# Kernel optimization log

Hardware: AMD Instinct MI355X
Metric: run time of the kernel (lower is better)

The kernel has to match this reference:

```python
import jax, jax.numpy as jnp
import numpy as np

B, S, E, H = 4, 2048, 1024, 16
D = E // H
EPS = 1e-5


def _ln(x, g, b):
    mu = jnp.mean(x, axis=-1, keepdims=True)
    var = jnp.mean(jnp.square(x - mu), axis=-1, keepdims=True)
    return (x - mu) * jax.lax.rsqrt(var + EPS) * g + b


def setup_inputs() -> dict:
    key = jax.random.key(0)
    ks = jax.random.split(key, 12)
    s = 0.02
    return {
        "inp": jax.random.normal(ks[0], (B, S, E), jnp.float32),
        "ln1_g": jnp.ones((E,), jnp.float32),
        "ln1_b": jnp.zeros((E,), jnp.float32),
        "Wq": jax.random.normal(ks[1], (E, E), jnp.float32) * s,
        "bq": jnp.zeros((E,), jnp.float32),
        "Wk": jax.random.normal(ks[2], (E, E), jnp.float32) * s,
        "bk": jnp.zeros((E,), jnp.float32),
        "Wv": jax.random.normal(ks[3], (E, E), jnp.float32) * s,
        "bv": jnp.zeros((E,), jnp.float32),
        "Wo": jax.random.normal(ks[4], (E, E), jnp.float32) * s,
        "bo": jnp.zeros((E,), jnp.float32),
        "ln2_g": jnp.ones((E,), jnp.float32),
        "ln2_b": jnp.zeros((E,), jnp.float32),
        "W1": jax.random.normal(ks[5], (E, 2 * E), jnp.float32) * s,
        "b1": jnp.zeros((2 * E,), jnp.float32),
        "W2": jax.random.normal(ks[6], (2 * E, E), jnp.float32) * s,
        "b2": jnp.zeros((E,), jnp.float32),
    }


def reference(inp, ln1_g, ln1_b, Wq, bq, Wk, bk, Wv, bv, Wo, bo,
              ln2_g, ln2_b, W1, b1, W2, b2):
    x = _ln(inp, ln1_g, ln1_b)                      # [B,S,E]
    def heads(t):
        return t.reshape(B, S, H, D).transpose(0, 2, 1, 3)  # [B,H,S,D]
    q = heads(x @ Wq + bq)
    k = heads(x @ Wk + bk)
    v = heads(x @ Wv + bv)
    scores = jnp.einsum('bhqd,bhkd->bhqk', q, k) / jnp.sqrt(jnp.float32(D))
    attn = jax.nn.softmax(scores, axis=-1)
    out = jnp.einsum('bhqk,bhkd->bhqd', attn, v)    # [B,H,S,D]
    out = out.transpose(0, 2, 1, 3).reshape(B, S, E)
    out = out @ Wo + bo                             # dropout p=1e-4 -> identity (eval)
    x = x + out                                     # NOTE: residual from normed input (as in source)
    x = _ln(x, ln2_g, ln2_b)
    mlp = jax.nn.gelu(x @ W1 + b1, approximate=False) @ W2 + b2
    return mlp + x
```

## Files before the change

kernel.cpp:

```cpp
#include <hip/hip_runtime.h>
#include <hip/hip_bf16.h>

typedef float f32x4 __attribute__((ext_vector_type(4)));
typedef __bf16 bfv8 __attribute__((ext_vector_type(8)));

constexpr int Bc = 4, Sc = 2048, Ec = 1024, Hc = 16, Dc = 64;
constexpr int Mc = Bc * Sc;

__device__ __forceinline__ uint pkbf(float lo, float hi) {
  uint r;
  asm("v_cvt_pk_bf16_f32 %0, %1, %2" : "=v"(r) : "v"(lo), "v"(hi));
  return r;
}
__device__ __forceinline__ ushort f2bf(float f) {
  __hip_bfloat16 h = __float2bfloat16(f);
  return __builtin_bit_cast(ushort, h);
}
__device__ __forceinline__ float bf2f(ushort u) {
  return __builtin_bit_cast(float, (uint)u << 16);
}

typedef __attribute__((address_space(1))) unsigned int as1_u32;
typedef __attribute__((address_space(3))) unsigned int as3_u32;
__device__ __forceinline__ void cp16(const ushort* g, ushort* l) {
  __builtin_amdgcn_global_load_lds((as1_u32*)g, (as3_u32*)l, 16, 0, 0);
}

__global__ __launch_bounds__(256) void wcvt_all_kernel(
    const float* __restrict__ Wq, const float* __restrict__ Wk,
    const float* __restrict__ Wv, const float* __restrict__ Wo,
    const float* __restrict__ W1, const float* __restrict__ W2,
    ushort* __restrict__ WqkvT, ushort* __restrict__ WoT,
    ushort* __restrict__ W1T, ushort* __restrict__ W2T) {
  int bid = blockIdx.x;
  const float* W;
  ushort* WT;
  int K, N;
  if (bid < 1024) {
    W = Wq; WT = WqkvT; K = 1024; N = 1024;
  } else if (bid < 2048) {
    W = Wk; WT = WqkvT + (size_t)1024 * 1024; K = 1024; N = 1024; bid -= 1024;
  } else if (bid < 3072) {
    W = Wv; WT = WqkvT + (size_t)2 * 1024 * 1024; K = 1024; N = 1024; bid -= 2048;
  } else if (bid < 4096) {
    W = Wo; WT = WoT; K = 1024; N = 1024; bid -= 3072;
  } else if (bid < 6144) {
    W = W1; WT = W1T; K = 1024; N = 2048; bid -= 4096;
  } else {
    W = W2; WT = W2T; K = 2048; N = 1024; bid -= 6144;
  }
  const int nbx = K / 32;
  const int k0 = (bid % nbx) * 32, n0 = (bid / nbx) * 32;
  __shared__ float t[32][33];
  int tx = threadIdx.x, ty = threadIdx.y;
#pragma unroll
  for (int i = 0; i < 32; i += 8)
    t[ty + i][tx] = W[(size_t)(k0 + ty + i) * N + n0 + tx];
  __syncthreads();
#pragma unroll
  for (int i = 0; i < 32; i += 8)
    WT[(size_t)(n0 + ty + i) * K + k0 + tx] = f2bf(t[tx][ty + i]);
}

template <int INF32>
__global__ __launch_bounds__(256) void ln_kernel(const void* in,
                                                 const float* __restrict__ g,
                                                 const float* __restrict__ bb,
                                                 ushort* ob) {
  int row = blockIdx.x;
  int t = threadIdx.x;
  float4 x;
  if constexpr (INF32) {
    x = reinterpret_cast<const float4*>((const float*)in + (size_t)row * Ec)[t];
  } else {
    uint2 u = reinterpret_cast<const uint2*>((const ushort*)in + (size_t)row * Ec)[t];
    x.x = __builtin_bit_cast(float, u.x << 16);
    x.y = __builtin_bit_cast(float, u.x & 0xFFFF0000u);
    x.z = __builtin_bit_cast(float, u.y << 16);
    x.w = __builtin_bit_cast(float, u.y & 0xFFFF0000u);
  }
  float s = x.x + x.y + x.z + x.w;
  float q = x.x * x.x + x.y * x.y + x.z * x.z + x.w * x.w;
#pragma unroll
  for (int o = 32; o > 0; o >>= 1) {
    s += __shfl_down(s, o);
    q += __shfl_down(q, o);
  }
  __shared__ float red[10];
  int wv = t >> 6;
  if ((t & 63) == 0) { red[wv] = s; red[4 + wv] = q; }
  __syncthreads();
  if (t == 0) {
    float S = red[0] + red[1] + red[2] + red[3];
    float Q = red[4] + red[5] + red[6] + red[7];
    float mu = S * (1.f / Ec);
    float var = Q * (1.f / Ec) - mu * mu;
    red[8] = mu;
    red[9] = rsqrtf(var + 1e-5f);
  }
  __syncthreads();
  float mu = red[8], rs = red[9];
  float4 gg = reinterpret_cast<const float4*>(g)[t];
  float4 b4 = reinterpret_cast<const float4*>(bb)[t];
  float4 y;
  y.x = (x.x - mu) * rs * gg.x + b4.x;
  y.y = (x.y - mu) * rs * gg.y + b4.y;
  y.z = (x.z - mu) * rs * gg.z + b4.z;
  y.w = (x.w - mu) * rs * gg.w + b4.w;
  uint2 u;
  u.x = pkbf(y.x, y.y);
  u.y = pkbf(y.z, y.w);
  reinterpret_cast<uint2*>(ob + (size_t)row * Ec)[t] = u;
}

template <int MODE>
__global__ __launch_bounds__(256, 2) void gemm_kernel(
    int M, int N, int K, const ushort* __restrict__ A,
    const ushort* __restrict__ BT, const float* __restrict__ b0,
    const ushort* __restrict__ rb, float* outF, ushort* o0, float qscale) {
  __shared__ __align__(16) ushort As[2][128 * 64];
  __shared__ __align__(16) ushort Bs[2][128 * 64];
  const int tid = threadIdx.x;
  const int lane = tid & 63, wave = tid >> 6;
  const int wr = wave >> 1, wc = wave & 1;
  const int fr = lane & 15, fq = lane >> 4;
  const int nx = gridDim.x;
  int flat = blockIdx.x + nx * blockIdx.y;
  int cpx = (nx * gridDim.y) >> 3;
  int work = (flat & 7) * cpx + (flat >> 3);
  const int n0 = (work % nx) * 128, m0 = (work / nx) * 128;

  f32x4 acc[4][4];
#pragma unroll
  for (int i = 0; i < 4; i++)
#pragma unroll
    for (int j = 0; j < 4; j++) acc[i][j] = f32x4{0.f, 0.f, 0.f, 0.f};

  const int srow = tid >> 3;
  const int sslot = tid & 7;

  auto STAGE = [&](int p, int k0) {
#pragma unroll
    for (int c = 0; c < 4; ++c) {
      int row = c * 32 + srow;
      int scol = (sslot ^ (row & 7)) * 8;
      cp16(A + (size_t)(m0 + row) * K + k0 + scol,
           &As[p][(c * 256 + wave * 64) * 8]);
      cp16(BT + (size_t)(n0 + row) * K + k0 + scol,
           &Bs[p][(c * 256 + wave * 64) * 8]);
    }
  };

  STAGE(0, 0);
  const int nt = K >> 6;
  for (int kt = 0; kt < nt; ++kt) {
    const int p = kt & 1;
    if (kt + 1 < nt) {
      STAGE(p ^ 1, (kt + 1) << 6);
      asm volatile("s_waitcnt vmcnt(8)" ::: "memory");
    } else {
      asm volatile("s_waitcnt vmcnt(0)" ::: "memory");
    }
    __builtin_amdgcn_s_barrier();
#pragma unroll
    for (int kk = 0; kk < 2; ++kk) {
      bfv8 af[4], bf[4];
#pragma unroll
      for (int m = 0; m < 4; m++) {
        int row = wr * 64 + m * 16 + fr;
        af[m] = *reinterpret_cast<const bfv8*>(
            &As[p][row * 64 + (((kk * 4 + fq) ^ (fr & 7)) * 8)]);
      }
#pragma unroll
      for (int n = 0; n < 4; n++) {
        int row = wc * 64 + n * 16 + fr;
        bf[n] = *reinterpret_cast<const bfv8*>(
            &Bs[p][row * 64 + (((kk * 4 + fq) ^ (fr & 7)) * 8)]);
      }
      __builtin_amdgcn_s_setprio(1);
#pragma unroll
      for (int m = 0; m < 4; m++)
#pragma unroll
        for (int n = 0; n < 4; n++)
          acc[m][n] =
              __builtin_amdgcn_mfma_f32_16x16x32_bf16(af[m], bf[n], acc[m][n], 0, 0, 0);
      __builtin_amdgcn_s_setprio(0);
    }
    __builtin_amdgcn_sched_barrier(0);
    __builtin_amdgcn_s_barrier();
  }

#pragma unroll
  for (int m = 0; m < 4; m++) {
#pragma unroll
    for (int n = 0; n < 4; n++) {
      const int row0 = m0 + wr * 64 + m * 16 + fq * 4;
      const int col = n0 + wc * 64 + n * 16 + fr;
      if constexpr (MODE == 0) {
        const int b = row0 >> 11, s0 = row0 & (Sc - 1);
        const int h = col >> 6, d = col & (Dc - 1);
        const float bb = b0[col];
#pragma unroll
        for (int r = 0; r < 4; r++)
          o0[(((size_t)b * Hc + h) * Sc + s0 + r) * Dc + d] =
              f2bf((acc[m][n][r] + bb) * qscale);
      } else {
        const float bb = b0[col];
#pragma unroll
        for (int r = 0; r < 4; r++) {
          int row = row0 + r;
          size_t idx = (size_t)row * N + col;
          float vacc = acc[m][n][r] + bb + bf2f(rb[idx]);
          if constexpr (MODE == 1) {
            o0[idx] = f2bf(vacc);
          } else {
            outF[idx] = vacc;
          }
        }
      }
    }
  }
}

template <int MODE>
__global__ __launch_bounds__(512, 2) void gemm256_kernel(
    int M, int N, int K, const ushort* __restrict__ A,
    const ushort* __restrict__ BT, const float* __restrict__ b0,
    const float* __restrict__ b1, ushort* o0, ushort* o1, float qscale) {
  __shared__ __align__(16) ushort As[2][256 * 64];
  __shared__ __align__(16) ushort Bs[2][256 * 64];
  const int tid = threadIdx.x;
  const int lane = tid & 63, wave = tid >> 6;
  const int wr = wave >> 2, wc = wave & 3;
  const int fr = lane & 15, fq = lane >> 4;
  const int nx = gridDim.x;
  int flat = blockIdx.x + nx * blockIdx.y;
  int cpx = (nx * gridDim.y) >> 3;
  int work = (flat & 7) * cpx + (flat >> 3);
  const int n0 = (work % nx) * 256, m0 = (work / nx) * 256;

  f32x4 acc[8][4];
#pragma unroll
  for (int i = 0; i < 8; i++)
#pragma unroll
    for (int j = 0; j < 4; j++) acc[i][j] = f32x4{0.f, 0.f, 0.f, 0.f};

  const int srow = tid >> 3;
  const int sslot = tid & 7;

  auto STAGE = [&](int p, int k0) {
#pragma unroll
    for (int c = 0; c < 4; ++c) {
      int row = c * 64 + srow;
      int scol = (sslot ^ (row & 7)) * 8;
      cp16(A + (size_t)(m0 + row) * K + k0 + scol,
           &As[p][(c * 64 + wave * 8) * 64]);
      cp16(BT + (size_t)(n0 + row) * K + k0 + scol,
           &Bs[p][(c * 64 + wave * 8) * 64]);
    }
  };

  STAGE(0, 0);
  const int nt = K >> 6;
  for (int kt = 0; kt < nt; ++kt) {
    const int p = kt & 1;
    if (kt + 1 < nt) {
      STAGE(p ^ 1, (kt + 1) << 6);
      asm volatile("s_waitcnt vmcnt(8)" ::: "memory");
    } else {
      asm volatile("s_waitcnt vmcnt(0)" ::: "memory");
    }
    __builtin_amdgcn_s_barrier();
#pragma unroll
    for (int kk = 0; kk < 2; ++kk) {
      bfv8 bfr[4];
#pragma unroll
      for (int n = 0; n < 4; ++n) {
        int row = wc * 64 + n * 16 + fr;
        bfr[n] = *reinterpret_cast<const bfv8*>(
            &Bs[p][row * 64 + (((kk * 4 + fq) ^ (row & 7)) * 8)]);
      }
#pragma unroll
      for (int mh = 0; mh < 2; ++mh) {
        bfv8 af[4];
#pragma unroll
        for (int mm = 0; mm < 4; ++mm) {
          int row = wr * 128 + (mh * 4 + mm) * 16 + fr;
          af[mm] = *reinterpret_cast<const bfv8*>(
              &As[p][row * 64 + (((kk * 4 + fq) ^ (row & 7)) * 8)]);
        }
        __builtin_amdgcn_s_setprio(1);
#pragma unroll
        for (int mm = 0; mm < 4; ++mm)
#pragma unroll
          for (int n = 0; n < 4; ++n)
            acc[mh * 4 + mm][n] = __builtin_amdgcn_mfma_f32_16x16x32_bf16(
                af[mm], bfr[n], acc[mh * 4 + mm][n], 0, 0, 0);
        __builtin_amdgcn_s_setprio(0);
        if (!(kk == 1 && mh == 1)) __builtin_amdgcn_s_barrier();
      }
    }
    __builtin_amdgcn_sched_barrier(0);
    __builtin_amdgcn_s_barrier();
  }

#pragma unroll
  for (int m = 0; m < 8; m++) {
#pragma unroll
    for (int n = 0; n < 4; n++) {
      const int row0 = m0 + wr * 128 + m * 16 + fq * 4;
      const int col = n0 + wc * 64 + n * 16 + fr;
      if constexpr (MODE == 2) {
        const float bb = b0[col];
#pragma unroll
        for (int r = 0; r < 4; r++) {
          float vacc = acc[m][n][r] + bb;
          vacc = 0.5f * vacc * (1.f + erff(vacc * 0.70710678118f));
          o0[(size_t)(row0 + r) * N + col] = f2bf(vacc);
        }
      } else {
        const int region = col >> 10, c1 = col & (Ec - 1);
        const int b = row0 >> 11, s0 = row0 & (Sc - 1);
        const int h = c1 >> 6, d = c1 & (Dc - 1);
        const float bb = (region ? b1 : b0)[c1];
        if (region == 1) {
          uint2 u;
          u.x = pkbf(acc[m][n][0] + bb, acc[m][n][1] + bb);
          u.y = pkbf(acc[m][n][2] + bb, acc[m][n][3] + bb);
          *reinterpret_cast<uint2*>(
              &o1[(((size_t)b * Hc + h) * Dc + d) * Sc + s0]) = u;
        } else {
#pragma unroll
          for (int r = 0; r < 4; r++)
            o0[(((size_t)b * Hc + h) * Sc + s0 + r) * Dc + d] =
                f2bf(acc[m][n][r] + bb);
        }
      }
    }
  }
}

__global__ __launch_bounds__(512) void attn_kernel(const ushort* __restrict__ q,
                                                   const ushort* __restrict__ k,
                                                   const ushort* __restrict__ vt,
                                                   ushort* __restrict__ o) {
  int flat = blockIdx.x;
  int swz = (flat & 7) * 128 + (flat >> 3);
  const int qb = swz & 15;
  const int bh = swz >> 4;
  const int tid = threadIdx.x, lane = tid & 63, wave = tid >> 6;
  const int fr = lane & 15, fq = lane >> 4;
  const size_t base = (size_t)bh * Sc * Dc;
  const int q0 = qb * 128 + wave * 16;

  __shared__ __align__(16) ushort Ks[2][128 * 64];
  __shared__ __align__(16) ushort Vt[2][64 * 128];
  __shared__ __align__(16) ushort Ps[8][16 * 64];

  bfv8 qf0, qf1;
  {
    const ushort* qp = q + base + (size_t)(q0 + fr) * Dc + fq * 8;
    qf0 = *reinterpret_cast<const bfv8*>(qp);
    qf1 = *reinterpret_cast<const bfv8*>(qp + 32);
  }

  const bfv8 ones = __builtin_bit_cast(bfv8, uint4{0x3F803F80u, 0x3F803F80u,
                                                  0x3F803F80u, 0x3F803F80u});

  f32x4 oacc[4];
  f32x4 oaccL;
  oaccL = f32x4{0.f, 0.f, 0.f, 0.f};
#pragma unroll
  for (int d = 0; d < 4; ++d) oacc[d] = f32x4{0.f, 0.f, 0.f, 0.f};

  const int rk = tid >> 3;
  const int ck = tid & 7;
  const int rv = tid >> 4;
  const int cv = tid & 15;

  auto STAGE = [&](int p, int key0) {
#pragma unroll
    for (int i = 0; i < 2; ++i) {
      int krow = i * 64 + rk;
      int skc = (ck ^ (krow & 7)) * 8;
      cp16(k + base + (size_t)(key0 + krow) * Dc + skc,
           &Ks[p][(i * 64 + wave * 8) * 64]);
    }
#pragma unroll
    for (int i = 0; i < 2; ++i) {
      int vrow = i * 32 + rv;
      int svc = (cv ^ (vrow & 15)) * 8;
      cp16(vt + base + (size_t)vrow * Sc + key0 + svc,
           &Vt[p][(i * 32 + wave * 4) * 128]);
    }
  };

  const int pswz = 2 * (fr & 7);
  const int pr0 = fr * 64 + ((fq * 2) ^ pswz) * 4;
  const int pr1 = fr * 64 + ((fq * 2 + 8) ^ pswz) * 4;

  STAGE(0, 0);
  constexpr int NT = Sc / 128;
  for (int kt = 0; kt < NT; ++kt) {
    const int p = kt & 1;
    if (kt + 1 < NT) {
      STAGE(p ^ 1, (kt + 1) * 128);
      asm volatile("s_waitcnt vmcnt(4)" ::: "memory");
    } else {
      asm volatile("s_waitcnt vmcnt(0)" ::: "memory");
    }
    __builtin_amdgcn_s_barrier();

#pragma unroll
    for (int h = 0; h < 2; ++h) {
      f32x4 sf[4];
      bfv8 kf0[4], kf1[4];
#pragma unroll
      for (int t = 0; t < 4; ++t) {
        int row = h * 64 + t * 16 + fr;
        kf0[t] = *reinterpret_cast<const bfv8*>(
            &Ks[p][row * 64 + ((fq ^ (row & 7)) * 8)]);
        kf1[t] = *reinterpret_cast<const bfv8*>(
            &Ks[p][row * 64 + (((4 + fq) ^ (row & 7)) * 8)]);
      }
      __builtin_amdgcn_s_setprio(1);
#pragma unroll
      for (int t = 0; t < 4; ++t) {
        sf[t] = f32x4{0.f, 0.f, 0.f, 0.f};
        sf[t] = __builtin_amdgcn_mfma_f32_16x16x32_bf16(kf0[t], qf0, sf[t], 0, 0, 0);
        sf[t] = __builtin_amdgcn_mfma_f32_16x16x32_bf16(kf1[t], qf1, sf[t], 0, 0, 0);
      }
      __builtin_amdgcn_s_setprio(0);
      ushort* pw = &Ps[wave][0];
#pragma unroll
      for (int t = 0; t < 4; ++t) {
        uint2 pu;
        pu.x = pkbf(__builtin_amdgcn_exp2f(sf[t][0]),
                    __builtin_amdgcn_exp2f(sf[t][1]));
        pu.y = pkbf(__builtin_amdgcn_exp2f(sf[t][2]),
                    __builtin_amdgcn_exp2f(sf[t][3]));
        int us = fr * 64 + ((t * 4 + fq) ^ pswz) * 4;
        *reinterpret_cast<uint2*>(&pw[us]) = pu;
      }
      bfv8 pf0 = *reinterpret_cast<const bfv8*>(&pw[pr0]);
      bfv8 pf1 = *reinterpret_cast<const bfv8*>(&pw[pr1]);
      bfv8 vf0[4], vf1[4];
#pragma unroll
      for (int t = 0; t < 4; ++t) {
        int row = t * 16 + fr;
        vf0[t] = *reinterpret_cast<const bfv8*>(
            &Vt[p][row * 128 + (((h * 8 + fq) ^ (row & 15)) * 8)]);
        vf1[t] = *reinterpret_cast<const bfv8*>(
            &Vt[p][row * 128 + (((h * 8 + 4 + fq) ^ (row & 15)) * 8)]);
      }
      __builtin_amdgcn_s_setprio(1);
#pragma unroll
      for (int d = 0; d < 4; ++d) {
        oacc[d] = __builtin_amdgcn_mfma_f32_16x16x32_bf16(pf0, vf0[d], oacc[d], 0, 0, 0);
        oacc[d] = __builtin_amdgcn_mfma_f32_16x16x32_bf16(pf1, vf1[d], oacc[d], 0, 0, 0);
      }
      oaccL = __builtin_amdgcn_mfma_f32_16x16x32_bf16(pf0, ones, oaccL, 0, 0, 0);
      oaccL = __builtin_amdgcn_mfma_f32_16x16x32_bf16(pf1, ones, oaccL, 0, 0, 0);
      __builtin_amdgcn_s_setprio(0);
    }

    __builtin_amdgcn_sched_barrier(0);
    __builtin_amdgcn_s_barrier();
  }

  const int b = bh >> 4, h = bh & 15;
  float linv[4];
#pragma unroll
  for (int r = 0; r < 4; ++r) linv[r] = 1.f / oaccL[r];
#pragma unroll
  for (int d = 0; d < 4; ++d)
#pragma unroll
    for (int r = 0; r < 4; ++r) {
      int sIdx = q0 + fq * 4 + r;
      o[((size_t)(b * Sc + sIdx)) * Ec + h * 64 + d * 16 + fr] =
          f2bf(oacc[d][r] * linv[r]);
    }
}

extern "C" void kernel_launch(void* const* d_in, const int* in_sizes, int n_in,
                              void* d_out, int out_size, void* d_ws, size_t ws_size,
                              hipStream_t stream) {
  const float* inp = (const float*)d_in[0];
  const float* ln1g = (const float*)d_in[1];
  const float* ln1b = (const float*)d_in[2];
  const float* Wq = (const float*)d_in[3];
  const float* bq = (const float*)d_in[4];
  const float* Wk = (const float*)d_in[5];
  const float* bk = (const float*)d_in[6];
  const float* Wv = (const float*)d_in[7];
  const float* bv = (const float*)d_in[8];
  const float* Wo = (const float*)d_in[9];
  const float* bo = (const float*)d_in[10];
  const float* ln2g = (const float*)d_in[11];
  const float* ln2b = (const float*)d_in[12];
  const float* W1 = (const float*)d_in[13];
  const float* b1 = (const float*)d_in[14];
  const float* W2 = (const float*)d_in[15];
  const float* b2 = (const float*)d_in[16];

  char* wsb = (char*)d_ws;
  size_t off = 0;
  auto alloc = [&](size_t bytes) {
    char* p = wsb + off;
    off += (bytes + 255) & ~(size_t)255;
    return p;
  };
  ushort* xb = (ushort*)alloc((size_t)Mc * Ec * 2);
  ushort* x2b = (ushort*)alloc((size_t)Mc * Ec * 2);
  ushort* x3b = (ushort*)alloc((size_t)Mc * Ec * 2);
  ushort* qbuf = (ushort*)alloc((size_t)Mc * Ec * 2);
  ushort* kbuf = (ushort*)alloc((size_t)Mc * Ec * 2);
  ushort* vtbuf = (ushort*)alloc((size_t)Mc * Ec * 2);
  ushort* abuf = (ushort*)alloc((size_t)Mc * Ec * 2);
  ushort* h1 = (ushort*)alloc((size_t)Mc * 2 * Ec * 2);
  ushort* WqkvT = (ushort*)alloc((size_t)3 * Ec * Ec * 2);
  ushort* WoT = (ushort*)alloc((size_t)Ec * Ec * 2);
  ushort* W1T = (ushort*)alloc((size_t)Ec * 2 * Ec * 2);
  ushort* W2T = (ushort*)alloc((size_t)Ec * 2 * Ec * 2);
  (void)in_sizes; (void)n_in; (void)out_size; (void)ws_size;

  wcvt_all_kernel<<<8192, dim3(32, 8), 0, stream>>>(Wq, Wk, Wv, Wo, W1, W2,
                                                    WqkvT, WoT, W1T, W2T);

  ln_kernel<1><<<Mc, 256, 0, stream>>>(inp, ln1g, ln1b, xb);

  gemm256_kernel<4><<<dim3(2 * Ec / 256, Mc / 256), 512, 0, stream>>>(
      Mc, 2 * Ec, Ec, xb, WqkvT + (size_t)Ec * Ec, bk, bv, kbuf, vtbuf, 1.f);

  gemm_kernel<0><<<dim3(Ec / 128, Mc / 128), 256, 0, stream>>>(
      Mc, Ec, Ec, xb, WqkvT, bq, nullptr, nullptr, qbuf, 0.18033688f);

  attn_kernel<<<Bc * Hc * (Sc / 128), 512, 0, stream>>>(qbuf, kbuf, vtbuf, abuf);

  gemm_kernel<1><<<dim3(Ec / 128, Mc / 128), 256, 0, stream>>>(
      Mc, Ec, Ec, abuf, WoT, bo, xb, nullptr, x2b, 1.f);

  ln_kernel<0><<<Mc, 256, 0, stream>>>(x2b, ln2g, ln2b, x3b);

  gemm256_kernel<2><<<dim3(2 * Ec / 256, Mc / 256), 512, 0, stream>>>(
      Mc, 2 * Ec, Ec, x3b, W1T, b1, nullptr, h1, nullptr, 1.f);

  gemm_kernel<3><<<dim3(Ec / 128, Mc / 128), 256, 0, stream>>>(
      Mc, Ec, 2 * Ec, h1, W2T, b2, x3b, (float*)d_out, nullptr, 1.f);
}
```

Measured before the change: 305.8 us.

## Switch attention to 32x32x16 MFMA with register-shuffled P and 256-query blocks

Rewrites the attention kernel to use 32x32x16 bf16 MFMA tiles, giving each wave 32 query rows instead of 16 and each block 256 queries. The P matrix is rearranged into A-operand layout with cross-lane shuffles instead of a round trip through LDS. The row sum is now accumulated in VALU rather than with an extra MFMA against ones. This halves the number of blocks, so K/V tiles staged in LDS are reused across twice as many queries, but it raises register pressure and uses fewer blocks on the device.

```diff
diff --git a/kernel.cpp b/kernel.cpp
--- a/kernel.cpp
+++ b/kernel.cpp
@@ -2,6 +2,7 @@
 #include <hip/hip_bf16.h>
 
 typedef float f32x4 __attribute__((ext_vector_type(4)));
+typedef float f32x16 __attribute__((ext_vector_type(16)));
 typedef __bf16 bfv8 __attribute__((ext_vector_type(8)));
 
 constexpr int Bc = 4, Sc = 2048, Ec = 1024, Hc = 16, Dc = 64;
@@ -345,33 +346,27 @@
                                                    const ushort* __restrict__ vt,
                                                    ushort* __restrict__ o) {
   int flat = blockIdx.x;
-  int swz = (flat & 7) * 128 + (flat >> 3);
-  const int qb = swz & 15;
-  const int bh = swz >> 4;
+  int swz = (flat & 7) * 64 + (flat >> 3);
+  const int qb = swz & 7;
+  const int bh = swz >> 3;
   const int tid = threadIdx.x, lane = tid & 63, wave = tid >> 6;
-  const int fr = lane & 15, fq = lane >> 4;
+  const int cq = lane & 31, hq = lane >> 5;
   const size_t base = (size_t)bh * Sc * Dc;
-  const int q0 = qb * 128 + wave * 16;
+  const int q0 = qb * 256 + wave * 32;
 
   __shared__ __align__(16) ushort Ks[2][128 * 64];
   __shared__ __align__(16) ushort Vt[2][64 * 128];
-  __shared__ __align__(16) ushort Ps[8][16 * 64];
-
-  bfv8 qf0, qf1;
-  {
-    const ushort* qp = q + base + (size_t)(q0 + fr) * Dc + fq * 8;
-    qf0 = *reinterpret_cast<const bfv8*>(qp);
-    qf1 = *reinterpret_cast<const bfv8*>(qp + 32);
-  }
-
-  const bfv8 ones = __builtin_bit_cast(bfv8, uint4{0x3F803F80u, 0x3F803F80u,
-                                                  0x3F803F80u, 0x3F803F80u});
-
-  f32x4 oacc[4];
-  f32x4 oaccL;
-  oaccL = f32x4{0.f, 0.f, 0.f, 0.f};
-#pragma unroll
-  for (int d = 0; d < 4; ++d) oacc[d] = f32x4{0.f, 0.f, 0.f, 0.f};
+
+  bfv8 qf[4];
+#pragma unroll
+  for (int dc = 0; dc < 4; ++dc)
+    qf[dc] = *reinterpret_cast<const bfv8*>(
+        q + base + (size_t)(q0 + cq) * Dc + dc * 16 + 8 * hq);
+
+  f32x16 oacc[2];
+  oacc[0] = 0.f;
+  oacc[1] = 0.f;
+  float lsum = 0.f;
 
   const int rk = tid >> 3;
   const int ck = tid & 7;
@@ -394,10 +389,6 @@
            &Vt[p][(i * 32 + wave * 4) * 128]);
     }
   };
-
-  const int pswz = 2 * (fr & 7);
-  const int pr0 = fr * 64 + ((fq * 2) ^ pswz) * 4;
-  const int pr1 = fr * 64 + ((fq * 2 + 8) ^ pswz) * 4;
 
   STAGE(0, 0);
   constexpr int NT = Sc / 128;
@@ -412,55 +403,49 @@
     __builtin_amdgcn_s_barrier();
 
 #pragma unroll
-    for (int h = 0; h < 2; ++h) {
-      f32x4 sf[4];
-      bfv8 kf0[4], kf1[4];
-#pragma unroll
-      for (int t = 0; t < 4; ++t) {
-        int row = h * 64 + t * 16 + fr;
-        kf0[t] = *reinterpret_cast<const bfv8*>(
-            &Ks[p][row * 64 + ((fq ^ (row & 7)) * 8)]);
-        kf1[t] = *reinterpret_cast<const bfv8*>(
-            &Ks[p][row * 64 + (((4 + fq) ^ (row & 7)) * 8)]);
-      }
+    for (int kb = 0; kb < 4; ++kb) {
+      bfv8 kf[4];
+#pragma unroll
+      for (int dc = 0; dc < 4; ++dc) {
+        int row = kb * 32 + cq;
+        kf[dc] = *reinterpret_cast<const bfv8*>(
+            &Ks[p][row * 64 + (((dc * 2 + hq) ^ (row & 7)) * 8)]);
+      }
+      f32x16 sf = 0.f;
       __builtin_amdgcn_s_setprio(1);
 #pragma unroll
-      for (int t = 0; t < 4; ++t) {
-        sf[t] = f32x4{0.f, 0.f, 0.f, 0.f};
-        sf[t] = __builtin_amdgcn_mfma_f32_16x16x32_bf16(kf0[t], qf0, sf[t], 0, 0, 0);
-        sf[t] = __builtin_amdgcn_mfma_f32_16x16x32_bf16(kf1[t], qf1, sf[t], 0, 0, 0);
-      }
+      for (int dc = 0; dc < 4; ++dc)
+        sf = __builtin_amdgcn_mfma_f32_32x32x16_bf16(kf[dc], qf[dc], sf, 0, 0, 0);
       __builtin_amdgcn_s_setprio(0);
-      ushort* pw = &Ps[wave][0];
-#pragma unroll
-      for (int t = 0; t < 4; ++t) {
-        uint2 pu;
-        pu.x = pkbf(__builtin_amdgcn_exp2f(sf[t][0]),
-                    __builtin_amdgcn_exp2f(sf[t][1]));
-        pu.y = pkbf(__builtin_amdgcn_exp2f(sf[t][2]),
-                    __builtin_amdgcn_exp2f(sf[t][3]));
-        int us = fr * 64 + ((t * 4 + fq) ^ pswz) * 4;
-        *reinterpret_cast<uint2*>(&pw[us]) = pu;
-      }
-      bfv8 pf0 = *reinterpret_cast<const bfv8*>(&pw[pr0]);
-      bfv8 pf1 = *reinterpret_cast<const bfv8*>(&pw[pr1]);
-      bfv8 vf0[4], vf1[4];
-#pragma unroll
-      for (int t = 0; t < 4; ++t) {
-        int row = t * 16 + fr;
-        vf0[t] = *reinterpret_cast<const bfv8*>(
-            &Vt[p][row * 128 + (((h * 8 + fq) ^ (row & 15)) * 8)]);
-        vf1[t] = *reinterpret_cast<const bfv8*>(
-            &Vt[p][row * 128 + (((h * 8 + 4 + fq) ^ (row & 15)) * 8)]);
-      }
+      float pv[16];
+#pragma unroll
+      for (int r = 0; r < 16; ++r) {
+        pv[r] = __builtin_amdgcn_exp2f(sf[r]);
+        lsum += pv[r];
+      }
+      uint pw[8], xw[8];
+#pragma unroll
+      for (int w = 0; w < 8; ++w) pw[w] = pkbf(pv[2 * w], pv[2 * w + 1]);
+#pragma unroll
+      for (int w = 0; w < 8; ++w) xw[w] = (uint)__shfl_xor((int)pw[w], 32);
+      const bool h = hq != 0;
+      uint4 a0{h ? xw[2] : pw[0], h ? xw[3] : pw[1],
+               h ? pw[2] : xw[0], h ? pw[3] : xw[1]};
+      uint4 a1{h ? xw[6] : pw[4], h ? xw[7] : pw[5],
+               h ? pw[6] : xw[4], h ? pw[7] : xw[5]};
+      bfv8 pa0 = __builtin_bit_cast(bfv8, a0);
+      bfv8 pa1 = __builtin_bit_cast(bfv8, a1);
       __builtin_amdgcn_s_setprio(1);
 #pragma unroll
-      for (int d = 0; d < 4; ++d) {
-        oacc[d] = __builtin_amdgcn_mfma_f32_16x16x32_bf16(pf0, vf0[d], oacc[d], 0, 0, 0);
-        oacc[d] = __builtin_amdgcn_mfma_f32_16x16x32_bf16(pf1, vf1[d], oacc[d], 0, 0, 0);
-      }
-      oaccL = __builtin_amdgcn_mfma_f32_16x16x32_bf16(pf0, ones, oaccL, 0, 0, 0);
-      oaccL = __builtin_amdgcn_mfma_f32_16x16x32_bf16(pf1, ones, oaccL, 0, 0, 0);
+      for (int dt = 0; dt < 2; ++dt) {
+        int row = dt * 32 + cq;
+        bfv8 v0 = *reinterpret_cast<const bfv8*>(
+            &Vt[p][row * 128 + (((kb * 4 + hq) ^ (row & 15)) * 8)]);
+        bfv8 v1 = *reinterpret_cast<const bfv8*>(
+            &Vt[p][row * 128 + (((kb * 4 + 2 + hq) ^ (row & 15)) * 8)]);
+        oacc[dt] = __builtin_amdgcn_mfma_f32_32x32x16_bf16(pa0, v0, oacc[dt], 0, 0, 0);
+        oacc[dt] = __builtin_amdgcn_mfma_f32_32x32x16_bf16(pa1, v1, oacc[dt], 0, 0, 0);
+      }
       __builtin_amdgcn_s_setprio(0);
     }
 
@@ -468,17 +453,19 @@
     __builtin_amdgcn_s_barrier();
   }
 
-  const int b = bh >> 4, h = bh & 15;
-  float linv[4];
-#pragma unroll
-  for (int r = 0; r < 4; ++r) linv[r] = 1.f / oaccL[r];
-#pragma unroll
-  for (int d = 0; d < 4; ++d)
-#pragma unroll
-    for (int r = 0; r < 4; ++r) {
-      int sIdx = q0 + fq * 4 + r;
-      o[((size_t)(b * Sc + sIdx)) * Ec + h * 64 + d * 16 + fr] =
-          f2bf(oacc[d][r] * linv[r]);
+  lsum += __shfl_xor(lsum, 32);
+  float linv = 1.f / lsum;
+
+  const int b = bh >> 4, hh = bh & 15;
+#pragma unroll
+  for (int dt = 0; dt < 2; ++dt)
+#pragma unroll
+    for (int r = 0; r < 16; ++r) {
+      int qrow = (r & 3) + 8 * (r >> 2) + 4 * hq;
+      float lr = __shfl(linv, qrow);
+      int sIdx = q0 + qrow;
+      o[((size_t)(b * Sc + sIdx)) * Ec + hh * 64 + dt * 32 + cq] =
+          f2bf(oacc[dt][r] * lr);
     }
 }
 
@@ -535,7 +522,7 @@
   gemm_kernel<0><<<dim3(Ec / 128, Mc / 128), 256, 0, stream>>>(
       Mc, Ec, Ec, xb, WqkvT, bq, nullptr, nullptr, qbuf, 0.18033688f);
 
-  attn_kernel<<<Bc * Hc * (Sc / 128), 512, 0, stream>>>(qbuf, kbuf, vtbuf, abuf);
+  attn_kernel<<<Bc * Hc * (Sc / 256), 512, 0, stream>>>(qbuf, kbuf, vtbuf, abuf);
 
   gemm_kernel<1><<<dim3(Ec / 128, Mc / 128), 256, 0, stream>>>(
       Mc, Ec, Ec, abuf, WoT, bo, xb, nullptr, x2b, 1.f);
```

Result: no change. 304.2 us (-0.5%).
